# Performance work log

Measured on AMD Instinct MI355X. Metric: run time of the kernel, lower is better.

## Reference

```python
import jax, jax.numpy as jnp
import numpy as np

EPS = 1e-5

def conv3x3(x, w, b=None):
    # NCHW, OIHW, stride 1, padding 1
    y = jax.lax.conv_general_dilated(x, w, (1, 1), ((1, 1), (1, 1)),
                                     dimension_numbers=('NCHW', 'OIHW', 'NCHW'))
    if b is not None:
        y = y + b[None, :, None, None]
    return y

def batchnorm(x, g, b):
    # training-mode BN (PyTorch default): biased variance over (N,H,W)
    m = x.mean((0, 2, 3), keepdims=True)
    v = x.var((0, 2, 3), keepdims=True)
    return (x - m) * jax.lax.rsqrt(v + EPS) * g[None, :, None, None] + b[None, :, None, None]

def upsample2x_align_corners(x):
    # bilinear, align_corners=True, scale_factor=2
    def lerp_axis(a, Lin, axis):
        Lout = 2 * Lin
        c = jnp.arange(Lout, dtype=a.dtype) * (Lin - 1) / (Lout - 1)
        i0 = jnp.floor(c).astype(jnp.int32)
        i1 = jnp.minimum(i0 + 1, Lin - 1)
        w = c - i0.astype(a.dtype)
        shape = [1] * a.ndim
        shape[axis] = Lout
        w = w.reshape(shape)
        return jnp.take(a, i0, axis=axis) * (1 - w) + jnp.take(a, i1, axis=axis) * w
    x = lerp_axis(x, x.shape[2], 2)
    x = lerp_axis(x, x.shape[3], 3)
    return x

def deform_sample(x, offsets):
    # torchvision DeformConv2d v1 sampling: kernel 3x3, pad 1, offsets [B,18,H,W]
    # layout: per kernel point k (row-major), channels (2k, 2k+1) = (dy, dx)
    B, C, H, W = x.shape
    K = 9
    off = offsets.reshape(B, K, 2, H, W)
    ky, kx = jnp.meshgrid(jnp.arange(3) - 1, jnp.arange(3) - 1, indexing='ij')
    ky = ky.reshape(K).astype(x.dtype)
    kx = kx.reshape(K).astype(x.dtype)
    gy = jnp.arange(H, dtype=x.dtype)[None, None, :, None]
    gx = jnp.arange(W, dtype=x.dtype)[None, None, None, :]
    py = gy + ky[None, :, None, None] + off[:, :, 0]  # [B,K,H,W]
    px = gx + kx[None, :, None, None] + off[:, :, 1]
    y0 = jnp.floor(py)
    x0 = jnp.floor(px)
    wy = (py - y0)[:, None]  # [B,1,K,H,W]
    wx = (px - x0)[:, None]
    y0i = y0.astype(jnp.int32)
    x0i = x0.astype(jnp.int32)
    x_flat = x.reshape(B, C, H * W)
    def gather(yi, xi):
        valid = ((yi >= 0) & (yi < H) & (xi >= 0) & (xi < W))
        idx = jnp.clip(yi, 0, H - 1) * W + jnp.clip(xi, 0, W - 1)  # [B,K,H,W]
        g = jnp.take_along_axis(x_flat, idx.reshape(B, 1, K * H * W), axis=2)
        return g.reshape(B, C, K, H, W) * valid[:, None].astype(x.dtype)
    v00 = gather(y0i, x0i)
    v01 = gather(y0i, x0i + 1)
    v10 = gather(y0i + 1, x0i)
    v11 = gather(y0i + 1, x0i + 1)
    return (v00 * (1 - wy) * (1 - wx) + v01 * (1 - wy) * wx
            + v10 * wy * (1 - wx) + v11 * wy * wx)

def setup_inputs() -> dict:
    key = jax.random.key(0)
    ks = jax.random.split(key, 6)
    B, in_ch, skip_ch, out_ch = 4, 256, 128, 128
    Hs, Ws = 128, 128
    x = jax.random.normal(ks[0], (B, in_ch, Hs // 2, Ws // 2), jnp.float32)
    skip = jax.random.normal(ks[1], (B, skip_ch, Hs, Ws), jnp.float32)
    cat_ch = in_ch + skip_ch
    conv1_w = jax.random.normal(ks[2], (out_ch, cat_ch, 3, 3), jnp.float32) * (2.0 / (cat_ch * 9)) ** 0.5
    off_w = jax.random.normal(ks[3], (18, out_ch, 3, 3), jnp.float32) * 0.01
    off_b = jnp.zeros((18,), jnp.float32)
    def_w = jax.random.normal(ks[4], (out_ch, out_ch, 3, 3), jnp.float32) * (2.0 / (out_ch * 9)) ** 0.5
    def_b = jnp.zeros((out_ch,), jnp.float32)
    return {
        'x': x, 'skip': skip,
        'conv1_w': conv1_w,
        'bn1_g': jnp.ones((out_ch,), jnp.float32), 'bn1_b': jnp.zeros((out_ch,), jnp.float32),
        'off_w': off_w, 'off_b': off_b,
        'def_w': def_w, 'def_b': def_b,
        'bn2_g': jnp.ones((out_ch,), jnp.float32), 'bn2_b': jnp.zeros((out_ch,), jnp.float32),
    }

def reference(x, skip, conv1_w, bn1_g, bn1_b, off_w, off_b, def_w, def_b, bn2_g, bn2_b):
    xu = upsample2x_align_corners(x)
    dh = skip.shape[2] - xu.shape[2]
    dw = skip.shape[3] - xu.shape[3]
    if dh != 0 or dw != 0:
        xu = jnp.pad(xu, ((0, 0), (0, 0), (dh // 2, dh - dh // 2), (dw // 2, dw - dw // 2)))
    cat = jnp.concatenate([skip, xu], axis=1)
    h = jax.nn.relu(batchnorm(conv3x3(cat, conv1_w), bn1_g, bn1_b))
    offsets = conv3x3(h, off_w, off_b)  # [B,18,H,W]
    sampled = deform_sample(h, offsets)  # [B,C,9,H,W]
    O = def_w.shape[0]
    y = jnp.einsum('ock,bckhw->bohw', def_w.reshape(O, def_w.shape[1], 9), sampled)
    y = y + def_b[None, :, None, None]
    return jax.nn.relu(batchnorm(y, bn2_g, bn2_b))
```

## Files before the change

kernel.cpp:

```cpp
#include <hip/hip_runtime.h>
#include <hip/hip_bf16.h>

typedef __hip_bfloat16 bf16;
typedef __bf16 bf16x8 __attribute__((ext_vector_type(8)));
typedef __bf16 bf16x4 __attribute__((ext_vector_type(4)));
typedef float  f32x4  __attribute__((ext_vector_type(4)));

constexpr int NB   = 4;
constexpr int H    = 128;
constexpr int W    = 128;
constexpr int HW   = H * W;
constexpr int NPIX = NB * HW;
constexpr int CCAT = 384;
constexpr int CSKIP= 128;
constexpr int CIN  = 256;
constexpr int CO   = 128;
constexpr int HS   = 64;
constexpr int WP   = 130;
constexpr int K1   = 3456;
constexpr int KD   = 1152;
constexpr int NBORD= 2 * WP + 2 * (WP - 2);
constexpr float EPS = 1e-5f;

__device__ __forceinline__ float b2f(bf16 v){ return __bfloat162float(v); }
__device__ __forceinline__ bf16  f2b(float v){ return __float2bfloat16(v); }

__device__ __forceinline__ void async_copy16(const void* g, void* s){
    __builtin_amdgcn_global_load_lds((const __attribute__((address_space(1))) void*)g,
                                     (__attribute__((address_space(3))) void*)s, 16, 0, 0);
}

__device__ __forceinline__ void border_yx(int p, int& y, int& x){
    if (p < WP)             { y = 0;        x = p; }
    else if (p < 2 * WP)    { y = WP - 1;   x = p - WP; }
    else if (p < 2 * WP + (WP - 2)) { y = p - 2 * WP + 1;          x = 0; }
    else                    { y = p - (2 * WP + (WP - 2)) + 1;     x = WP - 1; }
}

__global__ void k_prep(float* __restrict__ sums, bf16* __restrict__ catp,
                       bf16* __restrict__ hp){
    int i = blockIdx.x * blockDim.x + threadIdx.x;
    int stride = gridDim.x * blockDim.x;
    for (int j = i; j < 512; j += stride) sums[j] = 0.f;
    const int nCat = NB * NBORD * CCAT;
    for (int j = i; j < nCat; j += stride){
        int c = j % CCAT, r = j / CCAT, p = r % NBORD, b = r / NBORD;
        int y, x; border_yx(p, y, x);
        catp[(((size_t)b * WP + y) * WP + x) * CCAT + c] = f2b(0.f);
    }
    const int nHp = NB * NBORD * CO;
    for (int j = i; j < nHp; j += stride){
        int c = j % CO, r = j / CO, p = r % NBORD, b = r / NBORD;
        int y, x; border_yx(p, y, x);
        hp[(((size_t)b * WP + y) * WP + x) * CO + c] = f2b(0.f);
    }
}

__global__ __launch_bounds__(256) void k_build_cat2(const float* __restrict__ x,
                                                    const float* __restrict__ skip,
                                                    bf16* __restrict__ catp){
    constexpr int TS = 66;
    __shared__ bf16 tile[128 * TS];
    int t  = threadIdx.x;
    int y  = blockIdx.x % H, b = blockIdx.x / H;
    int xx = t & 127, cp = t >> 7;

    float cy = (y * 63.0f) / 127.0f;
    int   y0 = (int)cy;
    int   y1 = min(y0 + 1, HS - 1);
    float wy = cy - y0;
    float cxf = (xx * 63.0f) / 127.0f;
    int   x0 = (int)cxf;
    int   x1 = min(x0 + 1, HS - 1);
    float wx = cxf - x0;

    bf16* orow = catp + (((size_t)b * WP + y + 1) * WP + 1) * CCAT;

    for (int chunk = 0; chunk < 6; chunk++){
        int cbase = chunk * 64;
        if (chunk >= 1) __syncthreads();
        if (chunk < 2){
            const float* sb = skip + ((size_t)(b * CSKIP + cbase + cp * 32) * H + y) * W;
#pragma unroll
            for (int i = 0; i < 32; i++)
                tile[xx * TS + cp * 32 + i] = f2b(sb[(size_t)i * HW + xx]);
        } else {
            int icb = (chunk - 2) * 64 + cp * 32;
            const float* xr0 = x + ((size_t)(b * CIN + icb) * HS + y0) * HS;
            const float* xr1 = x + ((size_t)(b * CIN + icb) * HS + y1) * HS;
#pragma unroll
            for (int i = 0; i < 32; i++){
                const float* r0 = xr0 + (size_t)i * HS * HS;
                const float* r1 = xr1 + (size_t)i * HS * HS;
                float v0 = r0[x0] * (1 - wx) + r0[x1] * wx;
                float v1 = r1[x0] * (1 - wx) + r1[x1] * wx;
                tile[xx * TS + cp * 32 + i] = f2b(v0 * (1 - wy) + v1 * wy);
            }
        }
        __syncthreads();
        int cc2 = (t & 31) * 2;
        int px0 = t >> 5;
#pragma unroll
        for (int pp = 0; pp < 16; pp++){
            int px = pp * 8 + px0;
            unsigned int v = *(const unsigned int*)&tile[px * TS + cc2];
            *(unsigned int*)&orow[(size_t)px * CCAT + cbase + cc2] = v;
        }
    }
}

__global__ void k_tr_all(const float* __restrict__ w1, const float* __restrict__ wo,
                         const float* __restrict__ wd,
                         bf16* __restrict__ wt1, bf16* __restrict__ wto,
                         bf16* __restrict__ wtd){
    int i = blockIdx.x * blockDim.x + threadIdx.x;
    if (i < CO * K1){
        int k = i % K1, oc = i / K1;
        int ky = k / 1152, r = k % 1152, kx = r / 384, ic = r % 384;
        wt1[i] = f2b(w1[((oc * CCAT + ic) * 3 + ky) * 3 + kx]);
        return;
    }
    i -= CO * K1;
    if (i < 32 * KD){
        int kk = i % KD, o = i / KD;
        int ky = kk / 384, r = kk % 384, kx = r >> 7, ic = r & 127;
        wto[i] = (o < 18) ? f2b(wo[((o * CO + ic) * 3 + ky) * 3 + kx]) : f2b(0.f);
        return;
    }
    i -= 32 * KD;
    if (i < CO * KD){
        int kk = i % KD, o = i / KD;
        int kp = kk >> 7, c = kk & 127;
        wtd[i] = f2b(wd[(o * CO + c) * 9 + kp]);
    }
}

__global__ __launch_bounds__(256) void k_conv1_mfma(const bf16* __restrict__ catp,
                                                    const bf16* __restrict__ wbt,
                                                    bf16* __restrict__ hp,
                                                    float* __restrict__ sums){
    __shared__ unsigned short Ab[2][68 * 128];
    __shared__ unsigned short Bb[2][128 * 64];
    __shared__ float ps[256];
    int t = threadIdx.x;
    int l = t & 63, w = t >> 6;
    int half = blockIdx.x & 1;
    int y = (blockIdx.x >> 1) % H, b = blockIdx.x / (2 * H);
    int px0 = half * 64;

    int pr   = l >> 3;
    int koct = (l & 7) ^ pr;
    int m    = l & 15, quad = l >> 4;
    int wm   = w & 1,  wn   = w >> 1;

    f32x4 acc[2][4];
#pragma unroll
    for (int i = 0; i < 2; i++)
#pragma unroll
        for (int j = 0; j < 4; j++) acc[i][j] = f32x4{0.f, 0.f, 0.f, 0.f};

    const size_t rowStride = (size_t)WP * CCAT;

    {
        const bf16* Arow0 = catp + ((size_t)(b * WP) + y) * rowStride + (size_t)px0 * CCAT;
#pragma unroll
        for (int k = 0; k < 5; k++){
            int i = min(w + k * 4, 16);
            int G = i * 64 + l;
            int px = G >> 4, ol = G & 15;
            int osrc = ol ^ (px & 7);
            async_copy16(Arow0 + (size_t)px * CCAT + osrc * 8, &Ab[0][i * 512]);
        }
#pragma unroll
        for (int i = 0; i < 4; i++){
            int ocg = w * 32 + i * 8;
            async_copy16(wbt + (size_t)(ocg + pr) * K1 + koct * 8, &Bb[0][ocg * 64]);
        }
    }

    for (int p = 0; p < 54; p++){
        int g = p / 6;
        int j = p - g * 6;
        int s64 = j & 1, kx = j >> 1;

        __builtin_amdgcn_s_barrier();
        __builtin_amdgcn_sched_barrier(0);

        if (p < 53){
            int pn = p + 1;
            int gn = pn / 6, jn = pn - gn * 6;
            int kyn = gn / 3, cin = gn - kyn * 3;
            int kgn = kyn * 1152 + (jn >> 1) * 384 + cin * 128 + (jn & 1) * 64;
            int bufn = pn & 1;
#pragma unroll
            for (int i = 0; i < 4; i++){
                int ocg = w * 32 + i * 8;
                async_copy16(wbt + (size_t)(ocg + pr) * K1 + kgn + koct * 8,
                             &Bb[bufn][ocg * 64]);
            }
        }
        if (j == 1 && g < 8){
            int gn = g + 1;
            int kyn = gn / 3, cin = gn - kyn * 3;
            const bf16* Arow2 = catp + ((size_t)(b * WP) + y + kyn) * rowStride
                              + (size_t)px0 * CCAT + cin * 128;
#pragma unroll
            for (int k = 0; k < 5; k++){
                int i = min(w + k * 4, 16);
                int G = i * 64 + l;
                int px = G >> 4, ol = G & 15;
                int osrc = ol ^ (px & 7);
                async_copy16(Arow2 + (size_t)px * CCAT + osrc * 8, &Ab[gn & 1][i * 512]);
            }
        }
        if (p == 53)                              asm volatile("s_waitcnt vmcnt(0)" ::: "memory");
        else if ((j == 1 || j == 2) && g < 8)     asm volatile("s_waitcnt vmcnt(9)" ::: "memory");
        else                                      asm volatile("s_waitcnt vmcnt(4)" ::: "memory");
        __builtin_amdgcn_s_barrier();
        __builtin_amdgcn_sched_barrier(0);

        const bf16x8* ap = (const bf16x8*)&Ab[g & 1][0];
        const bf16x8* bp = (const bf16x8*)&Bb[p & 1][0];
        __builtin_amdgcn_s_setprio(1);
#pragma unroll
        for (int ks = 0; ks < 2; ks++){
            int s = s64 * 2 + ks;
            bf16x8 af[2], bfr[4];
#pragma unroll
            for (int mi = 0; mi < 2; mi++){
                int pxk = wm * 32 + mi * 16 + m + kx;
                af[mi] = ap[pxk * 16 + ((s * 4 + quad) ^ (pxk & 7))];
            }
#pragma unroll
            for (int ni = 0; ni < 4; ni++){
                int oc = wn * 64 + ni * 16 + m;
                bfr[ni] = bp[oc * 8 + ((ks * 4 + quad) ^ (oc & 7))];
            }
#pragma unroll
            for (int mi = 0; mi < 2; mi++)
#pragma unroll
                for (int ni = 0; ni < 4; ni++)
                    acc[mi][ni] = __builtin_amdgcn_mfma_f32_16x16x32_bf16(
                        af[mi], bfr[ni], acc[mi][ni], 0, 0, 0);
        }
        __builtin_amdgcn_s_setprio(0);
    }

    size_t obase = (((size_t)b * WP + y + 1) * WP + 1 + px0) * CO;
#pragma unroll
    for (int mi = 0; mi < 2; mi++){
        int p0 = wm * 32 + mi * 16 + quad * 4;
#pragma unroll
        for (int ni = 0; ni < 4; ni++){
            int oc = wn * 64 + ni * 16 + m;
#pragma unroll
            for (int r = 0; r < 4; r++)
                hp[obase + (size_t)(p0 + r) * CO + oc] = f2b(acc[mi][ni][r]);
        }
    }
    ps[t] = 0.f;
    __syncthreads();
#pragma unroll
    for (int ni = 0; ni < 4; ni++){
        int ch = wn * 64 + ni * 16 + m;
        float s = 0.f, q = 0.f;
#pragma unroll
        for (int mi = 0; mi < 2; mi++)
#pragma unroll
            for (int r = 0; r < 4; r++){
                float v = acc[mi][ni][r];
                s += v; q += v * v;
            }
        s += __shfl_xor(s, 16); s += __shfl_xor(s, 32);
        q += __shfl_xor(q, 16); q += __shfl_xor(q, 32);
        if (quad == 0){
            atomicAdd(&ps[ch], s);
            atomicAdd(&ps[128 + ch], q);
        }
    }
    __syncthreads();
    if (t < 128){
        atomicAdd(&sums[t],       ps[t]);
        atomicAdd(&sums[128 + t], ps[128 + t]);
    }
}

__global__ __launch_bounds__(256) void k_bn_apply_pad(bf16* __restrict__ t,
                                                      const float* __restrict__ sums,
                                                      const float* __restrict__ g,
                                                      const float* __restrict__ bb){
    __shared__ float ssc[256];
    int tt = threadIdx.x;
    if (tt < 128){
        float mean = sums[tt] / (float)NPIX;
        float var  = sums[128 + tt] / (float)NPIX - mean * mean;
        float scale = g[tt] * rsqrtf(var + EPS);
        ssc[tt]       = scale;
        ssc[128 + tt] = bb[tt] - mean * scale;
    }
    __syncthreads();
    int i = blockIdx.x * 256 + tt;
    if (i >= NPIX * CO) return;
    int c = i & 127;
    int pix = i >> 7;
    int xw = pix & 127, yh = (pix >> 7) & 127, b = pix >> 14;
    size_t a = (((size_t)b * WP + yh + 1) * WP + xw + 1) * CO + c;
    float v = b2f(t[a]) * ssc[c] + ssc[128 + c];
    t[a] = f2b(v > 0.f ? v : 0.f);
}

__global__ __launch_bounds__(256) void k_conv_off_mfma(const bf16* __restrict__ hp,
                                                       const bf16* __restrict__ wob,
                                                       const float* __restrict__ off_b,
                                                       bf16* __restrict__ offs){
    __shared__ unsigned short Ab[132 * 128];
    __shared__ unsigned short Bb[32 * 384];
    int t = threadIdx.x, l = t & 63, w = t >> 6;
    int y = blockIdx.x % H, b = blockIdx.x / H;
    int m = l & 15, quad = l >> 4;
    int wm = w & 1, wn = w >> 1;

    f32x4 acc[4];
#pragma unroll
    for (int i = 0; i < 4; i++) acc[i] = f32x4{0.f, 0.f, 0.f, 0.f};

    const size_t rowStrideH = (size_t)WP * CO;
    for (int ky = 0; ky < 3; ky++){
        const bf16* Arow = hp + ((size_t)(b * WP) + y + ky) * rowStrideH;
        __syncthreads();
        for (int i = w; i < 33; i += 4){
            int G  = i * 64 + l;
            int px = G >> 4, ol = G & 15;
            int osrc = ol ^ (px & 7);
            async_copy16(Arow + (size_t)px * CO + osrc * 8, &Ab[i * 512]);
        }
        for (int i = w; i < 24; i += 4){
            int g  = i * 64 + l;
            int kx = g >> 9, oc = (g >> 4) & 31, ol = g & 15;
            int osrc = ol ^ (oc & 7);
            async_copy16(wob + (size_t)oc * KD + ky * 384 + kx * 128 + osrc * 8,
                         &Bb[i * 512]);
        }
        __syncthreads();
        const bf16x8* ap = (const bf16x8*)Ab;
        const bf16x8* bp = (const bf16x8*)Bb;
        for (int kx = 0; kx < 3; kx++){
#pragma unroll
            for (int s = 0; s < 4; s++){
                int oc = wn * 16 + m;
                bf16x8 bfr = bp[kx * 512 + oc * 16 + ((s * 4 + quad) ^ (oc & 7))];
#pragma unroll
                for (int mi = 0; mi < 4; mi++){
                    int pxk = wm * 64 + mi * 16 + m + kx;
                    bf16x8 af = ap[pxk * 16 + ((s * 4 + quad) ^ (pxk & 7))];
                    acc[mi] = __builtin_amdgcn_mfma_f32_16x16x32_bf16(af, bfr, acc[mi], 0, 0, 0);
                }
            }
        }
    }
    int oc = wn * 16 + m;
    if (oc < 18){
        float bias = off_b[oc];
        int rowpix = b * HW + y * W;
#pragma unroll
        for (int mi = 0; mi < 4; mi++){
            int p0 = wm * 64 + mi * 16 + quad * 4;
#pragma unroll
            for (int r = 0; r < 4; r++)
                offs[(size_t)(rowpix + p0 + r) * 18 + oc] = f2b(acc[mi][r] + bias);
        }
    }
}

__global__ __launch_bounds__(256) void k_deform_mfma(const bf16* __restrict__ hp,
                                                     const bf16* __restrict__ offs,
                                                     const bf16* __restrict__ wdb,
                                                     const float* __restrict__ def_b,
                                                     bf16* __restrict__ y,
                                                     float* __restrict__ sums){
    __shared__ unsigned short Ab[128 * 64];
    __shared__ unsigned short Bb[128 * 64];
    __shared__ int2   sc_yx[9 * 128];
    __shared__ float4 sc_w[9 * 128];
    __shared__ float  ps[256];

    int t = threadIdx.x, l = t & 63, w = t >> 6;
    int yrow = blockIdx.x % H, b = blockIdx.x / H;
    int rowpix = b * HW + yrow * W;

    for (int idx = t; idx < 9 * 128; idx += 256){
        int kp = idx >> 7, px = idx & 127;
        float dy = b2f(offs[(size_t)(rowpix + px) * 18 + 2 * kp]);
        float dx = b2f(offs[(size_t)(rowpix + px) * 18 + 2 * kp + 1]);
        float py = yrow + (kp / 3 - 1) + dy;
        float pxx = px + (kp % 3 - 1) + dx;
        float fy = floorf(py), fx = floorf(pxx);
        float wy = py - fy, wx = pxx - fx;
        int y0 = (int)fy, x0 = (int)fx;
        bool vy0 = (y0 >= 0) && (y0 < H);
        bool vy1 = (y0 + 1 >= 0) && (y0 + 1 < H);
        bool vx0 = (x0 >= 0) && (x0 < W);
        bool vx1 = (x0 + 1 >= 0) && (x0 + 1 < W);
        int y0c = min(max(y0, 0), H - 1),     y1c = min(max(y0 + 1, 0), H - 1);
        int x0c = min(max(x0, 0), W - 1),     x1c = min(max(x0 + 1, 0), W - 1);
        sc_yx[idx] = make_int2(((y0c + 1) * WP) | (((y1c + 1) * WP) << 16),
                               (x0c + 1) | ((x1c + 1) << 16));
        sc_w[idx] = make_float4((1 - wy) * (1 - wx) * (float)(vy0 && vx0),
                                (1 - wy) * wx       * (float)(vy0 && vx1),
                                wy * (1 - wx)       * (float)(vy1 && vx0),
                                wy * wx             * (float)(vy1 && vx1));
    }
    __syncthreads();

    int pr = l >> 3, koct = (l & 7) ^ pr;
    int m = l & 15, quad = l >> 4;
    int wm = w & 1, wn = w >> 1;
    int g = l >> 4, j = l & 15;

    f32x4 acc[4][4];
#pragma unroll
    for (int i = 0; i < 4; i++)
#pragma unroll
        for (int jj = 0; jj < 4; jj++) acc[i][jj] = f32x4{0.f, 0.f, 0.f, 0.f};

    const bf16* hpb = hp + (size_t)b * WP * WP * CO;

    for (int kc = 0; kc < 18; kc++){
        int kp = kc >> 1, ch = (kc & 1) * 64;
        __syncthreads();
        int kg = kp * 128 + ch;
#pragma unroll
        for (int i = 0; i < 4; i++){
            int oc = w * 32 + i * 8 + pr;
            async_copy16(wdb + (size_t)oc * KD + kg + koct * 8,
                         &Bb[(w * 32 + i * 8) * 64]);
        }
        int cb = ch + j * 4;
#pragma unroll
        for (int p = 0; p < 8; p++){
            int px = w * 32 + g * 8 + p;
            int idx = kp * 128 + px;
            int2 yx = sc_yx[idx];
            float4 w4 = sc_w[idx];
            int r0 = yx.x & 0xffff, r1 = ((unsigned)yx.x) >> 16;
            int c0 = yx.y & 0xffff, c1 = ((unsigned)yx.y) >> 16;
            const bf16* base = hpb + cb;
            bf16x4 s00 = *(const bf16x4*)(base + (size_t)(r0 + c0) * CO);
            bf16x4 s01 = *(const bf16x4*)(base + (size_t)(r0 + c1) * CO);
            bf16x4 s10 = *(const bf16x4*)(base + (size_t)(r1 + c0) * CO);
            bf16x4 s11 = *(const bf16x4*)(base + (size_t)(r1 + c1) * CO);
            bf16x4 pv;
#pragma unroll
            for (int r = 0; r < 4; r++){
                float v = w4.x * (float)s00[r] + w4.y * (float)s01[r]
                        + w4.z * (float)s10[r] + w4.w * (float)s11[r];
                pv[r] = (__bf16)v;
            }
            int oct_sw = (j >> 1) ^ (px & 7);
            *(bf16x4*)&Ab[px * 64 + oct_sw * 8 + (j & 1) * 4] = pv;
        }
        __syncthreads();
        const bf16x8* ap = (const bf16x8*)Ab;
        const bf16x8* bp = (const bf16x8*)Bb;
#pragma unroll
        for (int ks = 0; ks < 2; ks++){
            bf16x8 af[4], bfr[4];
#pragma unroll
            for (int mi = 0; mi < 4; mi++){
                int px = wm * 64 + mi * 16 + m;
                af[mi] = ap[px * 8 + ((ks * 4 + quad) ^ (px & 7))];
            }
#pragma unroll
            for (int ni = 0; ni < 4; ni++){
                int oc = wn * 64 + ni * 16 + m;
                bfr[ni] = bp[oc * 8 + ((ks * 4 + quad) ^ (oc & 7))];
            }
#pragma unroll
            for (int mi = 0; mi < 4; mi++)
#pragma unroll
                for (int ni = 0; ni < 4; ni++)
                    acc[mi][ni] = __builtin_amdgcn_mfma_f32_16x16x32_bf16(
                        af[mi], bfr[ni], acc[mi][ni], 0, 0, 0);
        }
    }
#pragma unroll
    for (int mi = 0; mi < 4; mi++){
        int p0 = wm * 64 + mi * 16 + quad * 4;
#pragma unroll
        for (int ni = 0; ni < 4; ni++){
            int oc = wn * 64 + ni * 16 + m;
            float bias = def_b[oc];
#pragma unroll
            for (int r = 0; r < 4; r++)
                y[(size_t)(rowpix + p0 + r) * CO + oc] = f2b(acc[mi][ni][r] + bias);
        }
    }
    ps[t] = 0.f;
    __syncthreads();
#pragma unroll
    for (int ni = 0; ni < 4; ni++){
        int ch = wn * 64 + ni * 16 + m;
        float bias = def_b[ch];
        float s = 0.f, q = 0.f;
#pragma unroll
        for (int mi = 0; mi < 4; mi++)
#pragma unroll
            for (int r = 0; r < 4; r++){
                float v = acc[mi][ni][r] + bias;
                s += v; q += v * v;
            }
        s += __shfl_xor(s, 16); s += __shfl_xor(s, 32);
        q += __shfl_xor(q, 16); q += __shfl_xor(q, 32);
        if (quad == 0){
            atomicAdd(&ps[ch], s);
            atomicAdd(&ps[128 + ch], q);
        }
    }
    __syncthreads();
    if (t < 128){
        atomicAdd(&sums[t],       ps[t]);
        atomicAdd(&sums[128 + t], ps[128 + t]);
    }
}

__global__ __launch_bounds__(256) void k_final(const bf16* __restrict__ yb,
                                               const float* __restrict__ sums,
                                               const float* __restrict__ g,
                                               const float* __restrict__ bb,
                                               float* __restrict__ out){
    __shared__ unsigned short tile[128 * 129];
    __shared__ float ssc[256];
    int t = threadIdx.x;
    if (t < 128){
        float mean = sums[t] / (float)NPIX;
        float var  = sums[128 + t] / (float)NPIX - mean * mean;
        float scale = g[t] * rsqrtf(var + EPS);
        ssc[t]       = scale;
        ssc[128 + t] = bb[t] - mean * scale;
    }
    int yrow = blockIdx.x % H, b = blockIdx.x / H;
    int rowbase = b * HW + yrow * W;
    const unsigned short* src = (const unsigned short*)yb;
    for (int it = 0; it < 64; it++){
        int idx = it * 256 + t;
        int c = idx & 127, px = idx >> 7;
        tile[px * 129 + c] = src[(size_t)(rowbase + px) * CO + c];
    }
    __syncthreads();
    for (int it = 0; it < 64; it++){
        int idx = it * 256 + t;
        int xw = idx & 127, o = idx >> 7;
        unsigned short u = tile[xw * 129 + o];
        float v = (float)(*(const __bf16*)&u);
        v = v * ssc[o] + ssc[128 + o];
        out[(((size_t)b * CO + o) * H + yrow) * W + xw] = v > 0.f ? v : 0.f;
    }
}

extern "C" void kernel_launch(void* const* d_in, const int* in_sizes, int n_in,
                              void* d_out, int out_size, void* d_ws, size_t ws_size,
                              hipStream_t stream){
    const float* x      = (const float*)d_in[0];
    const float* skip   = (const float*)d_in[1];
    const float* conv1w = (const float*)d_in[2];
    const float* bn1g   = (const float*)d_in[3];
    const float* bn1b   = (const float*)d_in[4];
    const float* offw   = (const float*)d_in[5];
    const float* offb   = (const float*)d_in[6];
    const float* defw   = (const float*)d_in[7];
    const float* defb   = (const float*)d_in[8];
    const float* bn2g   = (const float*)d_in[9];
    const float* bn2b   = (const float*)d_in[10];
    float* out = (float*)d_out;

    char* ws = (char*)d_ws;
    size_t off_bytes = 0;
    auto alloc = [&](size_t bytes) -> void* {
        void* p = ws + off_bytes;
        off_bytes += (bytes + 255) & ~(size_t)255;
        return p;
    };
    const size_t catp_elems = (size_t)NB * WP * WP * CCAT;
    const size_t hp_elems   = (size_t)NB * WP * WP * CO;
    bf16*  catp  = (bf16*) alloc(catp_elems * 2 + 2048);
    bf16*  hp    = (bf16*) alloc(hp_elems * 2);
    bf16*  offs  = (bf16*) alloc((size_t)NPIX * 18 * 2);
    bf16*  yb    = (bf16*) alloc((size_t)NPIX * CO * 2);
    bf16*  wbt   = (bf16*) alloc((size_t)CO * K1 * 2);
    bf16*  wob   = (bf16*) alloc((size_t)32 * KD * 2);
    bf16*  wdb   = (bf16*) alloc((size_t)CO * KD * 2);
    float* sums  = (float*)alloc(512 * 4);
    float* sums1 = sums;
    float* sums2 = sums + 256;

    k_prep<<<1024, 256, 0, stream>>>(sums, catp, hp);

    k_build_cat2<<<NB * H, 256, 0, stream>>>(x, skip, catp);

    const int ntr = CO * K1 + 32 * KD + CO * KD;
    k_tr_all<<<(ntr + 255) / 256, 256, 0, stream>>>(conv1w, offw, defw, wbt, wob, wdb);

    k_conv1_mfma<<<NB * H * 2, 256, 0, stream>>>(catp, wbt, hp, sums1);

    k_bn_apply_pad<<<(NPIX * CO + 255) / 256, 256, 0, stream>>>(hp, sums1, bn1g, bn1b);

    k_conv_off_mfma<<<NB * H, 256, 0, stream>>>(hp, wob, offb, offs);

    k_deform_mfma<<<NB * H, 256, 0, stream>>>(hp, offs, wdb, defb, yb, sums2);

    k_final<<<NB * H, 256, 0, stream>>>(yb, sums2, bn2g, bn2b, out);
}
```

Before: 371.7 us.

## Deepen conv1 GEMM pipeline: prefetch weights two steps ahead, load fragments before barrier

Restructures the conv1 implicit-GEMM main loop so weight tiles are issued two iterations ahead instead of one. At the top of each iteration all LDS fragments for both k-substeps are read into registers before the barrier, so the copy into the freed buffer can start while the MFMAs run. The A-tile prefetch trigger and the vmcnt waits are shifted to match the new schedule. This adds register pressure and depends on the hand-tuned waitcnt values being correct.

```diff
diff --git a/kernel.cpp b/kernel.cpp
--- a/kernel.cpp
+++ b/kernel.cpp
@@ -176,31 +176,57 @@
             int ocg = w * 32 + i * 8;
             async_copy16(wbt + (size_t)(ocg + pr) * K1 + koct * 8, &Bb[0][ocg * 64]);
         }
-    }
-
+#pragma unroll
+        for (int i = 0; i < 4; i++){
+            int ocg = w * 32 + i * 8;
+            async_copy16(wbt + (size_t)(ocg + pr) * K1 + 64 + koct * 8, &Bb[1][ocg * 64]);
+        }
+        asm volatile("s_waitcnt vmcnt(4)" ::: "memory");
+        asm volatile("" ::: "memory");
+        __builtin_amdgcn_s_barrier();
+        asm volatile("" ::: "memory");
+    }
+
+#pragma unroll 1
     for (int p = 0; p < 54; p++){
-        int g = p / 6;
-        int j = p - g * 6;
-        int s64 = j & 1, kx = j >> 1;
-
+        int gp = p / 6, q = p - gp * 6;
+        int kx = q >> 1, s64 = q & 1;
+
+        const bf16x8* ap = (const bf16x8*)&Ab[gp & 1][0];
+        const bf16x8* bp = (const bf16x8*)&Bb[p & 1][0];
+        bf16x8 af[2][2], bfr[2][4];
+#pragma unroll
+        for (int ks = 0; ks < 2; ks++){
+            int s = s64 * 2 + ks;
+#pragma unroll
+            for (int mi = 0; mi < 2; mi++){
+                int pxk = wm * 32 + mi * 16 + m + kx;
+                af[ks][mi] = ap[pxk * 16 + ((s * 4 + quad) ^ (pxk & 7))];
+            }
+#pragma unroll
+            for (int ni = 0; ni < 4; ni++){
+                int oc = wn * 64 + ni * 16 + m;
+                bfr[ks][ni] = bp[oc * 8 + ((ks * 4 + quad) ^ (oc & 7))];
+            }
+        }
+        asm volatile("s_waitcnt lgkmcnt(0)" ::: "memory");
+        asm volatile("" ::: "memory");
         __builtin_amdgcn_s_barrier();
-        __builtin_amdgcn_sched_barrier(0);
-
-        if (p < 53){
-            int pn = p + 1;
-            int gn = pn / 6, jn = pn - gn * 6;
-            int kyn = gn / 3, cin = gn - kyn * 3;
-            int kgn = kyn * 1152 + (jn >> 1) * 384 + cin * 128 + (jn & 1) * 64;
-            int bufn = pn & 1;
+        asm volatile("" ::: "memory");
+
+        if (p < 52){
+            int T = p + 2;
+            int gT = T / 6, jT = T - gT * 6;
+            int kgn = (gT / 3) * 1152 + (jT >> 1) * 384 + (gT % 3) * 128 + (jT & 1) * 64;
 #pragma unroll
             for (int i = 0; i < 4; i++){
                 int ocg = w * 32 + i * 8;
                 async_copy16(wbt + (size_t)(ocg + pr) * K1 + kgn + koct * 8,
-                             &Bb[bufn][ocg * 64]);
-            }
-        }
-        if (j == 1 && g < 8){
-            int gn = g + 1;
+                             &Bb[T & 1][ocg * 64]);
+            }
+        }
+        if (q == 2 && gp < 8){
+            int gn = gp + 1;
             int kyn = gn / 3, cin = gn - kyn * 3;
             const bf16* Arow2 = catp + ((size_t)(b * WP) + y + kyn) * rowStride
                               + (size_t)px0 * CCAT + cin * 128;
@@ -213,37 +239,27 @@
                 async_copy16(Arow2 + (size_t)px * CCAT + osrc * 8, &Ab[gn & 1][i * 512]);
             }
         }
-        if (p == 53)                              asm volatile("s_waitcnt vmcnt(0)" ::: "memory");
-        else if ((j == 1 || j == 2) && g < 8)     asm volatile("s_waitcnt vmcnt(9)" ::: "memory");
-        else                                      asm volatile("s_waitcnt vmcnt(4)" ::: "memory");
-        __builtin_amdgcn_s_barrier();
-        __builtin_amdgcn_sched_barrier(0);
-
-        const bf16x8* ap = (const bf16x8*)&Ab[g & 1][0];
-        const bf16x8* bp = (const bf16x8*)&Bb[p & 1][0];
+
         __builtin_amdgcn_s_setprio(1);
 #pragma unroll
-        for (int ks = 0; ks < 2; ks++){
-            int s = s64 * 2 + ks;
-            bf16x8 af[2], bfr[4];
-#pragma unroll
-            for (int mi = 0; mi < 2; mi++){
-                int pxk = wm * 32 + mi * 16 + m + kx;
-                af[mi] = ap[pxk * 16 + ((s * 4 + quad) ^ (pxk & 7))];
-            }
-#pragma unroll
-            for (int ni = 0; ni < 4; ni++){
-                int oc = wn * 64 + ni * 16 + m;
-                bfr[ni] = bp[oc * 8 + ((ks * 4 + quad) ^ (oc & 7))];
-            }
+        for (int ks = 0; ks < 2; ks++)
 #pragma unroll
             for (int mi = 0; mi < 2; mi++)
 #pragma unroll
                 for (int ni = 0; ni < 4; ni++)
                     acc[mi][ni] = __builtin_amdgcn_mfma_f32_16x16x32_bf16(
-                        af[mi], bfr[ni], acc[mi][ni], 0, 0, 0);
-        }
+                        af[ks][mi], bfr[ks][ni], acc[mi][ni], 0, 0, 0);
         __builtin_amdgcn_s_setprio(0);
+
+        if (p < 53){
+            if (p == 52)                     asm volatile("s_waitcnt vmcnt(0)" ::: "memory");
+            else if ((q == 2 || q == 3) && gp < 8)
+                                             asm volatile("s_waitcnt vmcnt(9)" ::: "memory");
+            else                             asm volatile("s_waitcnt vmcnt(4)" ::: "memory");
+            asm volatile("" ::: "memory");
+            __builtin_amdgcn_s_barrier();
+            asm volatile("" ::: "memory");
+        }
     }
 
     size_t obase = (((size_t)b * WP + y + 1) * WP + 1 + px0) * CO;
@@ -263,19 +279,19 @@
 #pragma unroll
     for (int ni = 0; ni < 4; ni++){
         int ch = wn * 64 + ni * 16 + m;
-        float s = 0.f, q = 0.f;
+        float s = 0.f, q2 = 0.f;
 #pragma unroll
         for (int mi = 0; mi < 2; mi++)
 #pragma unroll
             for (int r = 0; r < 4; r++){
                 float v = acc[mi][ni][r];
-                s += v; q += v * v;
+                s += v; q2 += v * v;
             }
         s += __shfl_xor(s, 16); s += __shfl_xor(s, 32);
-        q += __shfl_xor(q, 16); q += __shfl_xor(q, 32);
+        q2 += __shfl_xor(q2, 16); q2 += __shfl_xor(q2, 32);
         if (quad == 0){
             atomicAdd(&ps[ch], s);
-            atomicAdd(&ps[128 + ch], q);
+            atomicAdd(&ps[128 + ch], q2);
         }
     }
     __syncthreads();
```

After: 358.9 us. 3.4% less time.
